# Performance work log

Measured on AMD Instinct MI355X. Metric: run time of the kernel, lower is better.

Reference implementation:

```python
import jax, jax.numpy as jnp
import numpy as np

H = 1024      # hidden_size
L = 2         # decoder_layers
V = 50257     # output_size (vocab)
S = 2048      # encoder seq_len (max_length)


def gru_cell(x, h, W_ih, W_hh, b_ih, b_hh):
    # x: [1, in], h: [1, H]; PyTorch GRU gate order: r, z, n
    gi = x @ W_ih.T + b_ih          # [1, 3H]
    gh = h @ W_hh.T + b_hh          # [1, 3H]
    i_r, i_z, i_n = jnp.split(gi, 3, axis=1)
    h_r, h_z, h_n = jnp.split(gh, 3, axis=1)
    r = jax.nn.sigmoid(i_r + h_r)
    z = jax.nn.sigmoid(i_z + h_z)
    n = jnp.tanh(i_n + r * h_n)
    return (1.0 - z) * n + z * h


def setup_inputs() -> dict:
    key = jax.random.key(0)
    ks = jax.random.split(key, 12)
    w = 0.02  # weight scale to keep activations sane
    return {
        "word_input": jax.random.randint(ks[0], (1,), 0, V, dtype=jnp.int64)
            if jax.config.jax_enable_x64 else jax.random.randint(ks[0], (1,), 0, V),
        "last_context": jax.random.normal(ks[1], (1, H), jnp.float32),
        "last_hidden": jax.random.normal(ks[2], (L, 1, H), jnp.float32),
        "encoder_outputs": jax.random.normal(ks[3], (S, 1, H), jnp.float32),
        "emb": jax.random.normal(ks[4], (V, H), jnp.float32) * w,
        "W_ih0": jax.random.normal(ks[5], (3 * H, 2 * H), jnp.float32) * w,
        "W_hh0": jax.random.normal(ks[6], (3 * H, H), jnp.float32) * w,
        "b_ih0": jnp.zeros((3 * H,), jnp.float32),
        "b_hh0": jnp.zeros((3 * H,), jnp.float32),
        "W_ih1": jax.random.normal(ks[7], (3 * H, H), jnp.float32) * w,
        "W_hh1": jax.random.normal(ks[8], (3 * H, H), jnp.float32) * w,
        "b_ih1": jnp.zeros((3 * H,), jnp.float32),
        "b_hh1": jnp.zeros((3 * H,), jnp.float32),
        "W_out": jax.random.normal(ks[9], (V, 2 * H), jnp.float32) * w,
        "b_out": jnp.zeros((V,), jnp.float32),
    }


def reference(word_input, last_context, last_hidden, encoder_outputs, emb,
              W_ih0, W_hh0, b_ih0, b_hh0, W_ih1, W_hh1, b_ih1, b_hh1,
              W_out, b_out):
    # embedding + concat with previous context -> GRU step input [1, 2H]
    word_embedded = emb[word_input]                       # [1, H]
    rnn_input = jnp.concatenate([word_embedded, last_context], axis=1)

    h0 = gru_cell(rnn_input, last_hidden[0], W_ih0, W_hh0, b_ih0, b_hh0)
    h1 = gru_cell(h0, last_hidden[1], W_ih1, W_hh1, b_ih1, b_hh1)
    hidden = jnp.stack([h0, h1], axis=0)                  # [L, 1, H]
    rnn_output = h1                                       # [1, H]

    # Attn 'general' in the source discards the Linear and uses a plain dot:
    enc = encoder_outputs[:, 0, :]                        # [S, H]
    energies = enc @ rnn_output[0]                        # [S]
    attn_weights = jax.nn.softmax(energies)[None, None, :]  # [1, 1, S]
    context = attn_weights[0] @ enc                       # [1, H]

    logits = jnp.concatenate([rnn_output, context], axis=1) @ W_out.T + b_out
    output = jax.nn.log_softmax(logits, axis=1)           # [1, V]
    return (output, context, hidden, attn_weights)
```

## Files before the change

### kernel.cpp

```cpp
#include <hip/hip_runtime.h>
#include <float.h>

#define H 1024
#define SEQ 2048
#define V 50257

#define OUT_CTX   50257
#define OUT_H0    (OUT_CTX + H)
#define OUT_H1    (OUT_H0 + H)
#define OUT_ATTN  (OUT_H1 + H)

#define WS_H0     0
#define WS_H1     1024
#define WS_E      2048
#define WS_EPM    4096
#define WS_EPS    4608
#define WS_CTX    5120
#define WS_LOGITS 6144
#define WS_LPM    56448
#define WS_LPS    57472
#define WS_LOGZ   58496

#define LOGITS_ROWS_PB 50
#define LOGITS_NB      ((V + LOGITS_ROWS_PB - 1) / LOGITS_ROWS_PB)

__device__ __forceinline__ float dot4(float4 a, float4 b) {
  return a.x * b.x + a.y * b.y + a.z * b.z + a.w * b.w;
}

__device__ __forceinline__ float wave_allreduce_sum(float v) {
  #pragma unroll
  for (int off = 32; off > 0; off >>= 1) v += __shfl_xor(v, off);
  return v;
}

__global__ __launch_bounds__(384) void gru0_kernel(
    const float* __restrict__ emb, const int* __restrict__ word,
    const float* __restrict__ last_context,
    const float* __restrict__ hprev,
    const float* __restrict__ W_ih,
    const float* __restrict__ W_hh,
    const float* __restrict__ b_ih, const float* __restrict__ b_hh,
    float* __restrict__ h_ws, float* __restrict__ h_out) {
  int j = blockIdx.x;
  int wave = threadIdx.x >> 6, lane = threadIdx.x & 63;
  __shared__ float parts[6];
  float acc = 0.0f;
  if (wave < 3) {
    const float4* wr = (const float4*)(W_ih + (size_t)(wave * H + j) * (2 * H));
    const float4* e4 = (const float4*)(emb + (size_t)word[0] * H);
    const float4* c4 = (const float4*)last_context;
    #pragma unroll
    for (int it = 0; it < 8; ++it) {
      int idx = it * 64 + lane;
      float4 xv = (it < 4) ? e4[idx] : c4[idx - 256];
      acc += dot4(wr[idx], xv);
    }
  } else {
    const float4* wr = (const float4*)(W_hh + (size_t)((wave - 3) * H + j) * H);
    const float4* hv = (const float4*)hprev;
    #pragma unroll
    for (int it = 0; it < 4; ++it) {
      int idx = it * 64 + lane;
      acc += dot4(wr[idx], hv[idx]);
    }
  }
  acc = wave_allreduce_sum(acc);
  if (lane == 0) parts[wave] = acc;
  __syncthreads();
  if (threadIdx.x == 0) {
    float gi_r = parts[0] + b_ih[j];
    float gi_z = parts[1] + b_ih[H + j];
    float gi_n = parts[2] + b_ih[2 * H + j];
    float gh_r = parts[3] + b_hh[j];
    float gh_z = parts[4] + b_hh[H + j];
    float gh_n = parts[5] + b_hh[2 * H + j];
    float r = 1.0f / (1.0f + expf(-(gi_r + gh_r)));
    float z = 1.0f / (1.0f + expf(-(gi_z + gh_z)));
    float n = tanhf(gi_n + r * gh_n);
    float hp = hprev[j];
    float hn = (1.0f - z) * n + z * hp;
    h_ws[j] = hn;
    h_out[j] = hn;
  }
}

__global__ __launch_bounds__(384) void gru1_kernel(
    const float* __restrict__ x,
    const float* __restrict__ hprev,
    const float* __restrict__ W_ih,
    const float* __restrict__ W_hh,
    const float* __restrict__ b_ih, const float* __restrict__ b_hh,
    float* __restrict__ h_ws, float* __restrict__ h_out) {
  int j = blockIdx.x;
  int wave = threadIdx.x >> 6, lane = threadIdx.x & 63;
  __shared__ float parts[6];
  const float* W   = (wave < 3) ? W_ih : W_hh;
  const float* vec = (wave < 3) ? x : hprev;
  int row = (wave < 3) ? wave : (wave - 3);
  const float4* wr = (const float4*)(W + (size_t)(row * H + j) * H);
  const float4* xv = (const float4*)vec;
  float acc = 0.0f;
  #pragma unroll
  for (int it = 0; it < 4; ++it) {
    int idx = it * 64 + lane;
    acc += dot4(wr[idx], xv[idx]);
  }
  acc = wave_allreduce_sum(acc);
  if (lane == 0) parts[wave] = acc;
  __syncthreads();
  if (threadIdx.x == 0) {
    float gi_r = parts[0] + b_ih[j];
    float gi_z = parts[1] + b_ih[H + j];
    float gi_n = parts[2] + b_ih[2 * H + j];
    float gh_r = parts[3] + b_hh[j];
    float gh_z = parts[4] + b_hh[H + j];
    float gh_n = parts[5] + b_hh[2 * H + j];
    float r = 1.0f / (1.0f + expf(-(gi_r + gh_r)));
    float z = 1.0f / (1.0f + expf(-(gi_z + gh_z)));
    float n = tanhf(gi_n + r * gh_n);
    float hp = hprev[j];
    float hn = (1.0f - z) * n + z * hp;
    h_ws[j] = hn;
    h_out[j] = hn;
  }
}

__global__ __launch_bounds__(256) void energies_kernel(
    const float* __restrict__ enc, const float* __restrict__ h1,
    float* __restrict__ energies, float* __restrict__ epm,
    float* __restrict__ eps, float* __restrict__ ctx) {
  int t = threadIdx.x;
  if (blockIdx.x < 4) ctx[blockIdx.x * 256 + t] = 0.0f;
  int wave = t >> 6, lane = t & 63;
  int s = blockIdx.x * 4 + wave;
  const float4* er = (const float4*)(enc + (size_t)s * H);
  const float4* hv = (const float4*)h1;
  float acc = 0.0f;
  #pragma unroll
  for (int it = 0; it < 4; ++it) {
    int idx = it * 64 + lane;
    acc += dot4(er[idx], hv[idx]);
  }
  acc = wave_allreduce_sum(acc);
  __shared__ float se[4];
  if (lane == 0) { se[wave] = acc; energies[s] = acc; }
  __syncthreads();
  if (t == 0) {
    float m = fmaxf(fmaxf(se[0], se[1]), fmaxf(se[2], se[3]));
    float ss = expf(se[0] - m) + expf(se[1] - m) + expf(se[2] - m) + expf(se[3] - m);
    epm[blockIdx.x] = m;
    eps[blockIdx.x] = ss;
  }
}

__global__ __launch_bounds__(256) void context_kernel(
    const float* __restrict__ energies, const float* __restrict__ epm,
    const float* __restrict__ eps, const float* __restrict__ enc,
    float* __restrict__ ctx, float* __restrict__ attn_out) {
  __shared__ float red[256];
  __shared__ float satt[32];
  int t = threadIdx.x;
  float m = fmaxf(epm[t], epm[t + 256]);
  red[t] = m;
  __syncthreads();
  #pragma unroll
  for (int off = 128; off > 0; off >>= 1) {
    if (t < off) red[t] = fmaxf(red[t], red[t + off]);
    __syncthreads();
  }
  float M = red[0];
  __syncthreads();
  red[t] = eps[t] * expf(epm[t] - M) + eps[t + 256] * expf(epm[t + 256] - M);
  __syncthreads();
  #pragma unroll
  for (int off = 128; off > 0; off >>= 1) {
    if (t < off) red[t] += red[t + off];
    __syncthreads();
  }
  float Zinv = 1.0f / red[0];
  int s0 = blockIdx.y * 32;
  if (t < 32) satt[t] = expf(energies[s0 + t] - M) * Zinv;
  __syncthreads();
  int h2 = blockIdx.x * 512 + t * 2;
  float a0 = 0.0f, a1 = 0.0f;
  for (int i = 0; i < 32; ++i) {
    float a = satt[i];
    float2 p = *(const float2*)(enc + (size_t)(s0 + i) * H + h2);
    a0 += a * p.x;
    a1 += a * p.y;
  }
  atomicAdd(&ctx[h2], a0);
  atomicAdd(&ctx[h2 + 1], a1);
  if (blockIdx.x == 0 && t < 32) attn_out[s0 + t] = satt[t];
}

__global__ __launch_bounds__(256) void logits_kernel(
    const float* __restrict__ W_out, const float* __restrict__ b_out,
    const float* __restrict__ h1, const float* __restrict__ ctx,
    float* __restrict__ logits, float* __restrict__ lpm,
    float* __restrict__ lps) {
  __shared__ float y[2 * H];
  __shared__ float wm[4], wsv[4];
  int t = threadIdx.x;
  #pragma unroll
  for (int i = 0; i < 4; ++i) {
    int k = t + i * 256;
    y[k] = h1[k];
    y[H + k] = ctx[k];
  }
  __syncthreads();
  int wave = t >> 6, lane = t & 63;
  const float4* yv = (const float4*)y;
  int base = blockIdx.x * LOGITS_ROWS_PB;
  int rend = min(base + LOGITS_ROWS_PB, V);
  float m = -FLT_MAX, s = 0.0f;
  int r = base + wave;
  for (; r + 4 < rend; r += 8) {
    const float4* w0 = (const float4*)(W_out + (size_t)r * (2 * H));
    const float4* w1 = (const float4*)(W_out + (size_t)(r + 4) * (2 * H));
    float a0 = 0.0f, a1 = 0.0f;
    #pragma unroll
    for (int it = 0; it < 8; ++it) {
      int idx = it * 64 + lane;
      float4 yy = yv[idx];
      a0 += dot4(w0[idx], yy);
      a1 += dot4(w1[idx], yy);
    }
    #pragma unroll
    for (int off = 32; off > 0; off >>= 1) {
      a0 += __shfl_xor(a0, off);
      a1 += __shfl_xor(a1, off);
    }
    float l0 = a0 + b_out[r];
    float l1 = a1 + b_out[r + 4];
    if (lane == 0) { logits[r] = l0; logits[r + 4] = l1; }
    float nm = fmaxf(m, fmaxf(l0, l1));
    s = s * expf(m - nm) + expf(l0 - nm) + expf(l1 - nm);
    m = nm;
  }
  for (; r < rend; r += 4) {
    const float4* w0 = (const float4*)(W_out + (size_t)r * (2 * H));
    float a0 = 0.0f;
    #pragma unroll
    for (int it = 0; it < 8; ++it) {
      int idx = it * 64 + lane;
      a0 += dot4(w0[idx], yv[idx]);
    }
    a0 = wave_allreduce_sum(a0);
    float l0 = a0 + b_out[r];
    if (lane == 0) logits[r] = l0;
    float nm = fmaxf(m, l0);
    s = s * expf(m - nm) + expf(l0 - nm);
    m = nm;
  }
  if (lane == 0) { wm[wave] = m; wsv[wave] = s; }
  __syncthreads();
  if (t == 0) {
    float mb = fmaxf(fmaxf(wm[0], wm[1]), fmaxf(wm[2], wm[3]));
    float sb = wsv[0] * expf(wm[0] - mb) + wsv[1] * expf(wm[1] - mb) +
               wsv[2] * expf(wm[2] - mb) + wsv[3] * expf(wm[3] - mb);
    lpm[blockIdx.x] = mb;
    lps[blockIdx.x] = sb;
  }
}

__global__ __launch_bounds__(256) void lse_final_kernel(
    const float* __restrict__ lpm, const float* __restrict__ lps,
    float* __restrict__ logZ) {
  __shared__ float red[256];
  int t = threadIdx.x;
  float m = -FLT_MAX;
  #pragma unroll
  for (int i = 0; i < 4; ++i) {
    int k = t + i * 256;
    if (k < LOGITS_NB) m = fmaxf(m, lpm[k]);
  }
  red[t] = m;
  __syncthreads();
  #pragma unroll
  for (int off = 128; off > 0; off >>= 1) {
    if (t < off) red[t] = fmaxf(red[t], red[t + off]);
    __syncthreads();
  }
  float M = red[0];
  __syncthreads();
  float s = 0.0f;
  #pragma unroll
  for (int i = 0; i < 4; ++i) {
    int k = t + i * 256;
    if (k < LOGITS_NB) s += lps[k] * expf(lpm[k] - M);
  }
  red[t] = s;
  __syncthreads();
  #pragma unroll
  for (int off = 128; off > 0; off >>= 1) {
    if (t < off) red[t] += red[t + off];
    __syncthreads();
  }
  if (t == 0) logZ[0] = M + logf(red[0]);
}

__global__ __launch_bounds__(256) void finalize_kernel(
    const float* __restrict__ logits, const float* __restrict__ logZ,
    const float* __restrict__ ctx, float* __restrict__ out) {
  int v = blockIdx.x * 256 + threadIdx.x;
  float lz = logZ[0];
  if (v < V) out[v] = logits[v] - lz;
  if (v < H) out[OUT_CTX + v] = ctx[v];
}

extern "C" void kernel_launch(void* const* d_in, const int* in_sizes, int n_in,
                              void* d_out, int out_size, void* d_ws, size_t ws_size,
                              hipStream_t stream) {
  const int*   word         = (const int*)d_in[0];
  const float* last_context = (const float*)d_in[1];
  const float* last_hidden  = (const float*)d_in[2];
  const float* enc          = (const float*)d_in[3];
  const float* emb          = (const float*)d_in[4];
  const float* W_ih0        = (const float*)d_in[5];
  const float* W_hh0        = (const float*)d_in[6];
  const float* b_ih0        = (const float*)d_in[7];
  const float* b_hh0        = (const float*)d_in[8];
  const float* W_ih1        = (const float*)d_in[9];
  const float* W_hh1        = (const float*)d_in[10];
  const float* b_ih1        = (const float*)d_in[11];
  const float* b_hh1        = (const float*)d_in[12];
  const float* W_out        = (const float*)d_in[13];
  const float* b_out        = (const float*)d_in[14];
  float* out = (float*)d_out;

  float* ws       = (float*)d_ws;
  float* h0       = ws + WS_H0;
  float* h1       = ws + WS_H1;
  float* energies = ws + WS_E;
  float* epm      = ws + WS_EPM;
  float* eps      = ws + WS_EPS;
  float* ctx      = ws + WS_CTX;
  float* logits   = ws + WS_LOGITS;
  float* lpm      = ws + WS_LPM;
  float* lps      = ws + WS_LPS;
  float* logZ     = ws + WS_LOGZ;

  gru0_kernel<<<H, 384, 0, stream>>>(emb, word, last_context, last_hidden,
                                     W_ih0, W_hh0, b_ih0, b_hh0, h0, out + OUT_H0);
  gru1_kernel<<<H, 384, 0, stream>>>(h0, last_hidden + H, W_ih1, W_hh1,
                                     b_ih1, b_hh1, h1, out + OUT_H1);
  energies_kernel<<<SEQ / 4, 256, 0, stream>>>(enc, h1, energies, epm, eps, ctx);
  context_kernel<<<dim3(2, 64), 256, 0, stream>>>(energies, epm, eps, enc, ctx,
                                                  out + OUT_ATTN);
  logits_kernel<<<LOGITS_NB, 256, 0, stream>>>(W_out, b_out, h1, ctx, logits,
                                               lpm, lps);
  lse_final_kernel<<<1, 256, 0, stream>>>(lpm, lps, logZ);
  finalize_kernel<<<(V + 255) / 256, 256, 0, stream>>>(logits, logZ, ctx, out);
}
```

Baseline: 691.2 us.

## Fuse energies with partial context via online softmax; merge logsumexp into finalize

The energies kernel now handles 16 encoder rows per block and, with block-local softmax weights, also computes a partial context vector from the rows it just read. This avoids the second pass over the encoder outputs and the atomics in the old context kernel. A small combine kernel rescales and sums the 128 partial contexts and writes the attention weights. The single-block logsumexp kernel is folded into finalize: every finalize block redundantly reduces the ~1006 block partials, which removes one launch at the cost of duplicated reduction work.

```diff
diff --git a/kernel.cpp b/kernel.cpp
--- a/kernel.cpp
+++ b/kernel.cpp
@@ -14,15 +14,17 @@
 #define WS_H1     1024
 #define WS_E      2048
 #define WS_EPM    4096
-#define WS_EPS    4608
-#define WS_CTX    5120
-#define WS_LOGITS 6144
-#define WS_LPM    56448
-#define WS_LPS    57472
-#define WS_LOGZ   58496
-
+#define WS_EPS    4224
+#define WS_PC     4352
+#define WS_CTX    135424
+#define WS_LOGITS 136448
+#define WS_LPM    186705
+#define WS_LPS    187711
+
+#define EBLK      16
+#define ENB       (SEQ / EBLK)
 #define LOGITS_ROWS_PB 50
-#define LOGITS_NB      ((V + LOGITS_ROWS_PB - 1) / LOGITS_ROWS_PB)
+#define LOGITS_NB ((V + LOGITS_ROWS_PB - 1) / LOGITS_ROWS_PB)
 
 __device__ __forceinline__ float dot4(float4 a, float4 b) {
   return a.x * b.x + a.y * b.y + a.z * b.z + a.w * b.w;
@@ -126,43 +128,60 @@
   }
 }
 
-__global__ __launch_bounds__(256) void energies_kernel(
+__global__ __launch_bounds__(256) void energies_pctx_kernel(
     const float* __restrict__ enc, const float* __restrict__ h1,
     float* __restrict__ energies, float* __restrict__ epm,
-    float* __restrict__ eps, float* __restrict__ ctx) {
+    float* __restrict__ eps, float* __restrict__ pctx) {
+  __shared__ float se[EBLK];
+  __shared__ float sw[EBLK];
   int t = threadIdx.x;
-  if (blockIdx.x < 4) ctx[blockIdx.x * 256 + t] = 0.0f;
   int wave = t >> 6, lane = t & 63;
-  int s = blockIdx.x * 4 + wave;
-  const float4* er = (const float4*)(enc + (size_t)s * H);
+  int s0 = blockIdx.x * EBLK;
   const float4* hv = (const float4*)h1;
-  float acc = 0.0f;
-  #pragma unroll
-  for (int it = 0; it < 4; ++it) {
-    int idx = it * 64 + lane;
-    acc += dot4(er[idx], hv[idx]);
-  }
-  acc = wave_allreduce_sum(acc);
-  __shared__ float se[4];
-  if (lane == 0) { se[wave] = acc; energies[s] = acc; }
+  #pragma unroll
+  for (int k = 0; k < 4; ++k) {
+    int s = s0 + wave * 4 + k;
+    const float4* er = (const float4*)(enc + (size_t)s * H);
+    float acc = 0.0f;
+    #pragma unroll
+    for (int it = 0; it < 4; ++it) {
+      int idx = it * 64 + lane;
+      acc += dot4(er[idx], hv[idx]);
+    }
+    acc = wave_allreduce_sum(acc);
+    if (lane == 0) { se[wave * 4 + k] = acc; energies[s] = acc; }
+  }
+  __syncthreads();
+  float mb = se[0];
+  #pragma unroll
+  for (int i = 1; i < EBLK; ++i) mb = fmaxf(mb, se[i]);
+  if (t < EBLK) sw[t] = expf(se[t] - mb);
   __syncthreads();
   if (t == 0) {
-    float m = fmaxf(fmaxf(se[0], se[1]), fmaxf(se[2], se[3]));
-    float ss = expf(se[0] - m) + expf(se[1] - m) + expf(se[2] - m) + expf(se[3] - m);
-    epm[blockIdx.x] = m;
-    eps[blockIdx.x] = ss;
-  }
-}
-
-__global__ __launch_bounds__(256) void context_kernel(
+    float sb = 0.0f;
+    #pragma unroll
+    for (int i = 0; i < EBLK; ++i) sb += sw[i];
+    epm[blockIdx.x] = mb;
+    eps[blockIdx.x] = sb;
+  }
+  float4 acc = make_float4(0.f, 0.f, 0.f, 0.f);
+  #pragma unroll
+  for (int i = 0; i < EBLK; ++i) {
+    float w = sw[i];
+    float4 p = ((const float4*)(enc + (size_t)(s0 + i) * H))[t];
+    acc.x += w * p.x; acc.y += w * p.y; acc.z += w * p.z; acc.w += w * p.w;
+  }
+  ((float4*)(pctx + (size_t)blockIdx.x * H))[t] = acc;
+}
+
+__global__ __launch_bounds__(256) void combine_kernel(
     const float* __restrict__ energies, const float* __restrict__ epm,
-    const float* __restrict__ eps, const float* __restrict__ enc,
-    float* __restrict__ ctx, float* __restrict__ attn_out) {
+    const float* __restrict__ eps, const float* __restrict__ pctx,
+    float* __restrict__ ctx, float* __restrict__ out) {
   __shared__ float red[256];
-  __shared__ float satt[32];
+  __shared__ float swg[ENB];
   int t = threadIdx.x;
-  float m = fmaxf(epm[t], epm[t + 256]);
-  red[t] = m;
+  red[t] = (t < ENB) ? epm[t] : -FLT_MAX;
   __syncthreads();
   #pragma unroll
   for (int off = 128; off > 0; off >>= 1) {
@@ -171,28 +190,27 @@
   }
   float M = red[0];
   __syncthreads();
-  red[t] = eps[t] * expf(epm[t] - M) + eps[t + 256] * expf(epm[t + 256] - M);
+  red[t] = (t < ENB) ? eps[t] * expf(epm[t] - M) : 0.0f;
   __syncthreads();
   #pragma unroll
   for (int off = 128; off > 0; off >>= 1) {
     if (t < off) red[t] += red[t + off];
     __syncthreads();
   }
-  float Zinv = 1.0f / red[0];
-  int s0 = blockIdx.y * 32;
-  if (t < 32) satt[t] = expf(energies[s0 + t] - M) * Zinv;
-  __syncthreads();
-  int h2 = blockIdx.x * 512 + t * 2;
-  float a0 = 0.0f, a1 = 0.0f;
-  for (int i = 0; i < 32; ++i) {
-    float a = satt[i];
-    float2 p = *(const float2*)(enc + (size_t)(s0 + i) * H + h2);
-    a0 += a * p.x;
-    a1 += a * p.y;
-  }
-  atomicAdd(&ctx[h2], a0);
-  atomicAdd(&ctx[h2 + 1], a1);
-  if (blockIdx.x == 0 && t < 32) attn_out[s0 + t] = satt[t];
+  float Z = red[0];
+  if (blockIdx.x < 4) {
+    if (t < ENB) swg[t] = expf(epm[t] - M) / Z;
+    __syncthreads();
+    int h = blockIdx.x * 256 + t;
+    float acc = 0.0f;
+    #pragma unroll 8
+    for (int b = 0; b < ENB; ++b) acc += swg[b] * pctx[(size_t)b * H + h];
+    ctx[h] = acc;
+    out[OUT_CTX + h] = acc;
+  } else {
+    int s = (blockIdx.x - 4) * 256 + t;
+    out[OUT_ATTN + s] = expf(energies[s] - M) / Z;
+  }
 }
 
 __global__ __launch_bounds__(256) void logits_kernel(
@@ -265,9 +283,9 @@
   }
 }
 
-__global__ __launch_bounds__(256) void lse_final_kernel(
-    const float* __restrict__ lpm, const float* __restrict__ lps,
-    float* __restrict__ logZ) {
+__global__ __launch_bounds__(256) void finalize_kernel(
+    const float* __restrict__ logits, const float* __restrict__ lpm,
+    const float* __restrict__ lps, float* __restrict__ out) {
   __shared__ float red[256];
   int t = threadIdx.x;
   float m = -FLT_MAX;
@@ -298,16 +316,9 @@
     if (t < off) red[t] += red[t + off];
     __syncthreads();
   }
-  if (t == 0) logZ[0] = M + logf(red[0]);
-}
-
-__global__ __launch_bounds__(256) void finalize_kernel(
-    const float* __restrict__ logits, const float* __restrict__ logZ,
-    const float* __restrict__ ctx, float* __restrict__ out) {
-  int v = blockIdx.x * 256 + threadIdx.x;
-  float lz = logZ[0];
-  if (v < V) out[v] = logits[v] - lz;
-  if (v < H) out[OUT_CTX + v] = ctx[v];
+  float logZ = M + logf(red[0]);
+  int v = blockIdx.x * 256 + t;
+  if (v < V) out[v] = logits[v] - logZ;
 }
 
 extern "C" void kernel_launch(void* const* d_in, const int* in_sizes, int n_in,
@@ -336,21 +347,19 @@
   float* energies = ws + WS_E;
   float* epm      = ws + WS_EPM;
   float* eps      = ws + WS_EPS;
+  float* pctx     = ws + WS_PC;
   float* ctx      = ws + WS_CTX;
   float* logits   = ws + WS_LOGITS;
   float* lpm      = ws + WS_LPM;
   float* lps      = ws + WS_LPS;
-  float* logZ     = ws + WS_LOGZ;
 
   gru0_kernel<<<H, 384, 0, stream>>>(emb, word, last_context, last_hidden,
                                      W_ih0, W_hh0, b_ih0, b_hh0, h0, out + OUT_H0);
   gru1_kernel<<<H, 384, 0, stream>>>(h0, last_hidden + H, W_ih1, W_hh1,
                                      b_ih1, b_hh1, h1, out + OUT_H1);
-  energies_kernel<<<SEQ / 4, 256, 0, stream>>>(enc, h1, energies, epm, eps, ctx);
-  context_kernel<<<dim3(2, 64), 256, 0, stream>>>(energies, epm, eps, enc, ctx,
-                                                  out + OUT_ATTN);
+  energies_pctx_kernel<<<ENB, 256, 0, stream>>>(enc, h1, energies, epm, eps, pctx);
+  combine_kernel<<<12, 256, 0, stream>>>(energies, epm, eps, pctx, ctx, out);
   logits_kernel<<<LOGITS_NB, 256, 0, stream>>>(W_out, b_out, h1, ctx, logits,
                                                lpm, lps);
-  lse_final_kernel<<<1, 256, 0, stream>>>(lpm, lps, logZ);
-  finalize_kernel<<<(V + 255) / 256, 256, 0, stream>>>(logits, logZ, ctx, out);
-}
+  finalize_kernel<<<(V + 255) / 256, 256, 0, stream>>>(logits, lpm, lps, out);
+}
```

Measured after the change: 690.4 us. No clear change (-0.1%).
